# Kernel optimization log

Measured on AMD Instinct MI355X. Metric: run time of the kernel, lower is better.

The kernel has to match this reference:

```python
import jax, jax.numpy as jnp
import numpy as np

N_NODES = 50000
N_EDGES = 1000000
NODE_F = 64
EDGE_F = 64
OUT_F = 128
K = 2  # matches init k=2


def setup_inputs() -> dict:
    key = jax.random.key(0)
    k1, k2, k3, k4, k5, k6 = jax.random.split(key, 6)
    node_feat = jax.random.normal(k1, (N_NODES, NODE_F), dtype=jnp.float32)
    edge_feat = jax.random.normal(k2, (N_EDGES, EDGE_F), dtype=jnp.float32)
    # nn.Linear(edge_feats*2 + node_feats, out_feats): weight [out, in], bias [out]
    W = jax.random.normal(k3, (OUT_F, 2 * EDGE_F + NODE_F), dtype=jnp.float32) * 0.05
    b = jax.random.normal(k4, (OUT_F,), dtype=jnp.float32) * 0.05
    src = jax.random.randint(k5, (N_EDGES,), 0, N_NODES, dtype=jnp.int64)
    dst = jax.random.randint(k6, (N_EDGES,), 0, N_NODES, dtype=jnp.int64)
    return {"node_feat": node_feat, "edge_feat": edge_feat, "W": W, "b": b,
            "src": src, "dst": dst}


def reference(node_feat, edge_feat, W, b, src, dst):
    N = node_feat.shape[0]
    # norm = in_degrees().clamp(min=1) ** -0.5, shape [N, 1]
    deg = jax.ops.segment_sum(jnp.ones_like(dst, dtype=node_feat.dtype), dst,
                              num_segments=N)
    norm = jnp.maximum(deg, 1.0) ** -0.5
    norm = norm[:, None]
    # DGL semantics: update_all(copy_e, sum) overwrites ndata['h'] with the
    # scatter-sum of edge data over destination nodes; apply_edges then copies
    # the (un-normalized) node 'h' back to edges via edge.src.
    e = edge_feat  # [E, EDGE_F]
    fstack = [node_feat]
    for _ in range(K):
        h = jax.ops.segment_sum(e, dst, num_segments=N)  # [N, EDGE_F]
        fstack.append(h * norm)
        e = h[src]  # apply_edges: e = src node h (un-normalized)
    rst = jnp.concatenate(fstack, axis=-1) @ W.T + b  # [N, OUT_F]
    est = rst[src]  # final apply_edges copies lin output to edges
    return rst, est
```

## Files before the change

kernel.cpp:

```cpp
#include <hip/hip_runtime.h>
#include <hip/hip_bf16.h>

#define NF 64
#define N_OUT 128
#define CAT 192

typedef __attribute__((ext_vector_type(4))) float f32x4;
typedef __attribute__((ext_vector_type(8))) short bf16x8;

__device__ inline short f2bf(float x) {
  unsigned u = __float_as_uint(x);
  unsigned r = (u + 0x7fff + ((u >> 16) & 1)) >> 16;
  return (short)r;
}

__device__ inline f32x4 sx4(f32x4 v, int m) {
  f32x4 r;
  r.x = __shfl_xor(v.x, m, 64);
  r.y = __shfl_xor(v.y, m, 64);
  r.z = __shfl_xor(v.z, m, 64);
  r.w = __shfl_xor(v.w, m, 64);
  return r;
}

__global__ __launch_bounds__(256) void deg_kernel(const int* __restrict__ dst,
                                                  int* __restrict__ deg, int n_edges) {
  int i = blockIdx.x * blockDim.x + threadIdx.x;
  int stride = gridDim.x * blockDim.x;
  for (; i < n_edges; i += stride) {
    int d = __builtin_nontemporal_load(&dst[i]);
    atomicAdd(&deg[d], 1);
  }
}

__global__ __launch_bounds__(256) void scanA_kernel(const int* __restrict__ deg,
                                                    int* __restrict__ offs,
                                                    float* __restrict__ norm,
                                                    int* __restrict__ bsum, int n) {
  int tid = threadIdx.x;
  int i = blockIdx.x * 256 + tid;
  int lane = tid & 63, wid = tid >> 6;
  int v = (i < n) ? deg[i] : 0;
  int s = v;
  #pragma unroll
  for (int o = 1; o < 64; o <<= 1) {
    int t = __shfl_up(s, o, 64);
    if (lane >= o) s += t;
  }
  __shared__ int ws[4], wb[4];
  if (lane == 63) ws[wid] = s;
  __syncthreads();
  if (tid == 0) {
    int run = 0;
    #pragma unroll
    for (int w = 0; w < 4; ++w) { wb[w] = run; run += ws[w]; }
    bsum[blockIdx.x] = run;
  }
  __syncthreads();
  if (i < n) {
    offs[i] = wb[wid] + s - v;
    norm[i] = rsqrtf(fmaxf((float)v, 1.0f));
  }
}

__global__ __launch_bounds__(256) void scanBC_kernel(const int* __restrict__ bsum,
                                                     int* __restrict__ offs, int n, int nb) {
  int tid = threadIdx.x, lane = tid & 63, wid = tid >> 6;
  int v = (tid < nb) ? bsum[tid] : 0;
  int s = v;
  #pragma unroll
  for (int o = 1; o < 64; o <<= 1) {
    int t = __shfl_up(s, o, 64);
    if (lane >= o) s += t;
  }
  __shared__ int ws[4], wb[4];
  if (lane == 63) ws[wid] = s;
  __syncthreads();
  if (tid == 0) {
    int run = 0;
    #pragma unroll
    for (int w = 0; w < 4; ++w) { wb[w] = run; run += ws[w]; }
  }
  __syncthreads();
  __shared__ int sbase;
  if (tid == blockIdx.x) sbase = wb[wid] + s - v;
  __syncthreads();
  int i = blockIdx.x * 256 + tid;
  if (i < n) offs[i] += sbase;
}

__global__ __launch_bounds__(256) void fill_kernel(const int* __restrict__ src,
                                                   const int* __restrict__ dst,
                                                   int* __restrict__ offs,
                                                   long long* __restrict__ csr, int n_edges) {
  int i = blockIdx.x * blockDim.x + threadIdx.x;
  int stride = gridDim.x * blockDim.x;
  for (; i < n_edges; i += stride) {
    int d = __builtin_nontemporal_load(&dst[i]);
    int s = __builtin_nontemporal_load(&src[i]);
    int p = atomicAdd(&offs[d], 1);
    long long pk = (long long)(((unsigned long long)(unsigned)s << 32) | (unsigned)i);
    __builtin_nontemporal_store(pk, &csr[p]);
  }
}

__global__ __launch_bounds__(256) void h1_kernel(const float* __restrict__ edge_feat,
                                                 const int2* __restrict__ csr,
                                                 const int* __restrict__ offs,
                                                 float* __restrict__ h1, int n_nodes) {
  int n = blockIdx.x * 4 + (threadIdx.x >> 6);
  if (n >= n_nodes) return;
  int l = threadIdx.x & 63;
  int l15 = l & 15, l4 = l >> 4;
  int kb = n ? offs[n - 1] : 0;
  int ke = offs[n];
  f32x4 acc0 = {0.f,0.f,0.f,0.f}, acc1 = {0.f,0.f,0.f,0.f};
  f32x4 acc2 = {0.f,0.f,0.f,0.f}, acc3 = {0.f,0.f,0.f,0.f};
  int k = kb;
  for (; k + 16 <= ke; k += 16) {
    int e0 = csr[k + l4].x;
    int e1 = csr[k + 4 + l4].x;
    int e2 = csr[k + 8 + l4].x;
    int e3 = csr[k + 12 + l4].x;
    acc0 += __builtin_nontemporal_load((const f32x4*)&edge_feat[(size_t)e0 * NF + l15 * 4]);
    acc1 += __builtin_nontemporal_load((const f32x4*)&edge_feat[(size_t)e1 * NF + l15 * 4]);
    acc2 += __builtin_nontemporal_load((const f32x4*)&edge_feat[(size_t)e2 * NF + l15 * 4]);
    acc3 += __builtin_nontemporal_load((const f32x4*)&edge_feat[(size_t)e3 * NF + l15 * 4]);
  }
  if (k + 8 <= ke) {
    int e0 = csr[k + l4].x;
    int e1 = csr[k + 4 + l4].x;
    acc0 += __builtin_nontemporal_load((const f32x4*)&edge_feat[(size_t)e0 * NF + l15 * 4]);
    acc1 += __builtin_nontemporal_load((const f32x4*)&edge_feat[(size_t)e1 * NF + l15 * 4]);
    k += 8;
  }
  if (k + 4 <= ke) {
    int e = csr[k + l4].x;
    acc2 += __builtin_nontemporal_load((const f32x4*)&edge_feat[(size_t)e * NF + l15 * 4]);
    k += 4;
  }
  int rem = ke - k;
  if (l4 < rem) {
    int e = csr[k + l4].x;
    acc3 += __builtin_nontemporal_load((const f32x4*)&edge_feat[(size_t)e * NF + l15 * 4]);
  }
  f32x4 t = (acc0 + acc1) + (acc2 + acc3);
  t += sx4(t, 16);
  t += sx4(t, 32);
  if (l4 == 0) *(f32x4*)&h1[(size_t)n * NF + l15 * 4] = t;
}

__global__ __launch_bounds__(256) void h2_kernel(const float* __restrict__ h1,
                                                 const int2* __restrict__ csr,
                                                 const int* __restrict__ offs,
                                                 float* __restrict__ h2, int n_nodes) {
  int n = blockIdx.x * 4 + (threadIdx.x >> 6);
  if (n >= n_nodes) return;
  int l = threadIdx.x & 63;
  int l15 = l & 15, l4 = l >> 4;
  int kb = n ? offs[n - 1] : 0;
  int ke = offs[n];
  f32x4 acc0 = {0.f,0.f,0.f,0.f}, acc1 = {0.f,0.f,0.f,0.f};
  f32x4 acc2 = {0.f,0.f,0.f,0.f}, acc3 = {0.f,0.f,0.f,0.f};
  int k = kb;
  for (; k + 16 <= ke; k += 16) {
    int s0 = csr[k + l4].y;
    int s1 = csr[k + 4 + l4].y;
    int s2 = csr[k + 8 + l4].y;
    int s3 = csr[k + 12 + l4].y;
    acc0 += *(const f32x4*)&h1[(size_t)s0 * NF + l15 * 4];
    acc1 += *(const f32x4*)&h1[(size_t)s1 * NF + l15 * 4];
    acc2 += *(const f32x4*)&h1[(size_t)s2 * NF + l15 * 4];
    acc3 += *(const f32x4*)&h1[(size_t)s3 * NF + l15 * 4];
  }
  if (k + 8 <= ke) {
    int s0 = csr[k + l4].y;
    int s1 = csr[k + 4 + l4].y;
    acc0 += *(const f32x4*)&h1[(size_t)s0 * NF + l15 * 4];
    acc1 += *(const f32x4*)&h1[(size_t)s1 * NF + l15 * 4];
    k += 8;
  }
  if (k + 4 <= ke) {
    int s = csr[k + l4].y;
    acc2 += *(const f32x4*)&h1[(size_t)s * NF + l15 * 4];
    k += 4;
  }
  int rem = ke - k;
  if (l4 < rem) {
    int s = csr[k + l4].y;
    acc3 += *(const f32x4*)&h1[(size_t)s * NF + l15 * 4];
  }
  f32x4 t = (acc0 + acc1) + (acc2 + acc3);
  t += sx4(t, 16);
  t += sx4(t, 32);
  if (l4 == 0) *(f32x4*)&h2[(size_t)n * NF + l15 * 4] = t;
}

__global__ __launch_bounds__(512) void gemm_kernel(const float* __restrict__ node_feat,
                                                   const float* __restrict__ h1,
                                                   const float* __restrict__ h2,
                                                   const float* __restrict__ norm,
                                                   const float* __restrict__ W,
                                                   const float* __restrict__ bias,
                                                   float* __restrict__ rst,
                                                   short* __restrict__ rstb, int n_nodes) {
  __shared__ short F[64 * 200];
  __shared__ float R[64][132];
  int tid = threadIdx.x;
  int l = tid & 63, w = tid >> 6;
  int w2 = w & 3, wh = w >> 2;
  int l15 = l & 15, l4 = l >> 4;

  bf16x8 Bf[6][2];
  #pragma unroll
  for (int c = 0; c < 2; ++c) {
    int col = w2 * 32 + c * 16 + l15;
    const float* wp = &W[(size_t)col * CAT];
    #pragma unroll
    for (int ks = 0; ks < 6; ++ks) {
      int k0 = ks * 32 + l4 * 8;
      bf16x8 b;
      #pragma unroll
      for (int j = 0; j < 8; ++j) b[j] = f2bf(wp[k0 + j]);
      Bf[ks][c] = b;
    }
  }
  float bias0 = bias[w2 * 32 + l15];
  float bias1 = bias[w2 * 32 + 16 + l15];

  int tiles = (n_nodes + 63) / 64;
  for (int tile = blockIdx.x; tile < tiles; tile += gridDim.x) {
    int nbase = tile * 64;
    __syncthreads();
    for (int idx = tid; idx < 1536; idx += 512) {
      int m = idx / 24, q = idx - m * 24;
      int n = nbase + m;
      bf16x8 pk;
      if (n < n_nodes) {
        const float* sp;
        float scale = 1.f;
        if (q < 8)       sp = &node_feat[(size_t)n * NF + q * 8];
        else if (q < 16) { sp = &h1[(size_t)n * NF + (q - 8) * 8]; scale = norm[n]; }
        else             { sp = &h2[(size_t)n * NF + (q - 16) * 8]; scale = norm[n]; }
        f32x4 v0 = *(const f32x4*)sp;
        f32x4 v1 = *(const f32x4*)(sp + 4);
        pk[0] = f2bf(v0.x * scale); pk[1] = f2bf(v0.y * scale);
        pk[2] = f2bf(v0.z * scale); pk[3] = f2bf(v0.w * scale);
        pk[4] = f2bf(v1.x * scale); pk[5] = f2bf(v1.y * scale);
        pk[6] = f2bf(v1.z * scale); pk[7] = f2bf(v1.w * scale);
      } else {
        pk = bf16x8{0,0,0,0,0,0,0,0};
      }
      *(bf16x8*)&F[m * 200 + q * 8] = pk;
    }
    __syncthreads();
    f32x4 acc00 = {0.f,0.f,0.f,0.f}, acc01 = {0.f,0.f,0.f,0.f};
    f32x4 acc10 = {0.f,0.f,0.f,0.f}, acc11 = {0.f,0.f,0.f,0.f};
    #pragma unroll
    for (int ks = 0; ks < 6; ++ks) {
      bf16x8 a0 = *(const bf16x8*)&F[(wh * 32 + l15) * 200 + ks * 32 + l4 * 8];
      bf16x8 a1 = *(const bf16x8*)&F[(wh * 32 + 16 + l15) * 200 + ks * 32 + l4 * 8];
      acc00 = __builtin_amdgcn_mfma_f32_16x16x32_bf16(a0, Bf[ks][0], acc00, 0, 0, 0);
      acc01 = __builtin_amdgcn_mfma_f32_16x16x32_bf16(a0, Bf[ks][1], acc01, 0, 0, 0);
      acc10 = __builtin_amdgcn_mfma_f32_16x16x32_bf16(a1, Bf[ks][0], acc10, 0, 0, 0);
      acc11 = __builtin_amdgcn_mfma_f32_16x16x32_bf16(a1, Bf[ks][1], acc11, 0, 0, 0);
    }
    #pragma unroll
    for (int rt = 0; rt < 2; ++rt) {
      f32x4 ac0 = rt ? acc10 : acc00;
      f32x4 ac1 = rt ? acc11 : acc01;
      #pragma unroll
      for (int r = 0; r < 4; ++r) {
        int row = wh * 32 + rt * 16 + l4 * 4 + r;
        R[row][w2 * 32 + l15] = ac0[r] + bias0;
        R[row][w2 * 32 + 16 + l15] = ac1[r] + bias1;
      }
    }
    __syncthreads();
    for (int idx = tid; idx < 64 * 32; idx += 512) {
      int m = idx >> 5, c = idx & 31;
      int n = nbase + m;
      if (n < n_nodes) {
        f32x4 v = *(const f32x4*)&R[m][c * 4];
        __builtin_nontemporal_store(v, (f32x4*)&rst[(size_t)n * N_OUT + c * 4]);
      }
    }
    if (rstb) {
      for (int idx = tid; idx < 64 * 16; idx += 512) {
        int m = idx >> 4, q = idx & 15;
        int n = nbase + m;
        if (n < n_nodes) {
          const float* rp = &R[m][q * 8];
          bf16x8 pk;
          #pragma unroll
          for (int j = 0; j < 8; ++j) pk[j] = f2bf(rp[j]);
          *(bf16x8*)&rstb[(size_t)n * N_OUT + q * 8] = pk;
        }
      }
    }
  }
}

__global__ __launch_bounds__(256) void est_bf16_kernel(const short* __restrict__ rstb,
                                                       const int* __restrict__ src,
                                                       float* __restrict__ est, int n_edges) {
  f32x4* e4 = (f32x4*)est;
  int total = n_edges * 32;
  int i = blockIdx.x * blockDim.x + threadIdx.x;
  int stride = gridDim.x * blockDim.x;
  for (; i < total; i += stride) {
    int e = i >> 5, c = i & 31;
    ushort4 b = *(const ushort4*)&rstb[(size_t)src[e] * N_OUT + c * 4];
    f32x4 v;
    v.x = __uint_as_float((unsigned)b.x << 16);
    v.y = __uint_as_float((unsigned)b.y << 16);
    v.z = __uint_as_float((unsigned)b.z << 16);
    v.w = __uint_as_float((unsigned)b.w << 16);
    __builtin_nontemporal_store(v, &e4[i]);
  }
}

__global__ __launch_bounds__(256) void est_f32_kernel(const float* __restrict__ rst,
                                                      const int* __restrict__ src,
                                                      float* __restrict__ est, int n_edges) {
  const f32x4* r4 = (const f32x4*)rst;
  f32x4* e4 = (f32x4*)est;
  int total = n_edges * 32;
  int i = blockIdx.x * blockDim.x + threadIdx.x;
  int stride = gridDim.x * blockDim.x;
  for (; i < total; i += stride) {
    int e = i >> 5, c = i & 31;
    f32x4 v = r4[(size_t)src[e] * 32 + c];
    __builtin_nontemporal_store(v, &e4[i]);
  }
}

extern "C" void kernel_launch(void* const* d_in, const int* in_sizes, int n_in,
                              void* d_out, int out_size, void* d_ws, size_t ws_size,
                              hipStream_t stream) {
  const float* node_feat = (const float*)d_in[0];
  const float* edge_feat = (const float*)d_in[1];
  const float* W = (const float*)d_in[2];
  const float* bias = (const float*)d_in[3];
  const int* src = (const int*)d_in[4];
  const int* dst = (const int*)d_in[5];
  int n_nodes = in_sizes[0] / NF;
  int n_edges = in_sizes[4];

  size_t off = 0;
  auto take = [&](size_t bytes) -> void* {
    void* p = (char*)d_ws + off;
    off += (bytes + 255) & ~(size_t)255;
    return p;
  };
  int* deg = (int*)take((size_t)n_nodes * 4);
  int* offs = (int*)take(((size_t)n_nodes + 1) * 4);
  float* norm = (float*)take((size_t)n_nodes * 4);
  int* bsum = (int*)take(256 * 4);
  long long* csr = (long long*)take((size_t)n_edges * 8);
  float* h1 = (float*)take((size_t)n_nodes * NF * 4);
  float* h2 = (float*)take((size_t)n_nodes * NF * 4);
  size_t rstb_bytes = (size_t)n_nodes * N_OUT * 2;
  short* rstb = nullptr;
  if (off + rstb_bytes <= ws_size) rstb = (short*)take(rstb_bytes);

  float* rst = (float*)d_out;
  float* est = rst + (size_t)n_nodes * N_OUT;

  (void)hipMemsetAsync(deg, 0, (size_t)n_nodes * 4, stream);

  deg_kernel<<<2048, 256, 0, stream>>>(dst, deg, n_edges);
  int nbs = (n_nodes + 255) / 256;
  scanA_kernel<<<nbs, 256, 0, stream>>>(deg, offs, norm, bsum, n_nodes);
  scanBC_kernel<<<nbs, 256, 0, stream>>>(bsum, offs, n_nodes, nbs);
  fill_kernel<<<2048, 256, 0, stream>>>(src, dst, offs, csr, n_edges);
  int nb = (n_nodes + 3) / 4;
  h1_kernel<<<nb, 256, 0, stream>>>(edge_feat, (const int2*)csr, offs, h1, n_nodes);
  h2_kernel<<<nb, 256, 0, stream>>>(h1, (const int2*)csr, offs, h2, n_nodes);
  gemm_kernel<<<512, 512, 0, stream>>>(node_feat, h1, h2, norm, W, bias,
                                       rst, rstb, n_nodes);
  if (rstb)
    est_bf16_kernel<<<8192, 256, 0, stream>>>(rstb, src, est, n_edges);
  else
    est_f32_kernel<<<8192, 256, 0, stream>>>(rst, src, est, n_edges);
}
```

Measured before the change: 382.8 us.

## Store intermediate node features in bf16 and prenormalize before GEMM

The first aggregation kernel now writes h1 as bf16 twice, once raw and once scaled by norm, and also converts node_feat to bf16. The second aggregation kernel gathers the bf16 raw h1 and writes a normalized bf16 h2. The GEMM then loads pre-packed bf16 tiles directly instead of converting fp32 with scaling. The goal is to halve the gather traffic in h2 and the GEMM's load bytes. In exchange, h1 is rounded to bf16 before the second aggregation, which adds error, and the fp32 fallback for est is removed, so the bf16 workspace is assumed always to fit.

```diff
diff --git a/kernel.cpp b/kernel.cpp
--- a/kernel.cpp
+++ b/kernel.cpp
@@ -8,10 +8,25 @@
 typedef __attribute__((ext_vector_type(4))) float f32x4;
 typedef __attribute__((ext_vector_type(8))) short bf16x8;
 
-__device__ inline short f2bf(float x) {
+__device__ inline unsigned short f2bf(float x) {
   unsigned u = __float_as_uint(x);
   unsigned r = (u + 0x7fff + ((u >> 16) & 1)) >> 16;
-  return (short)r;
+  return (unsigned short)r;
+}
+
+__device__ inline ushort4 pack4(f32x4 v) {
+  ushort4 r;
+  r.x = f2bf(v.x); r.y = f2bf(v.y); r.z = f2bf(v.z); r.w = f2bf(v.w);
+  return r;
+}
+
+__device__ inline f32x4 unpack4(ushort4 b) {
+  f32x4 v;
+  v.x = __uint_as_float((unsigned)b.x << 16);
+  v.y = __uint_as_float((unsigned)b.y << 16);
+  v.z = __uint_as_float((unsigned)b.z << 16);
+  v.w = __uint_as_float((unsigned)b.w << 16);
+  return v;
 }
 
 __device__ inline f32x4 sx4(f32x4 v, int m) {
@@ -105,9 +120,14 @@
 }
 
 __global__ __launch_bounds__(256) void h1_kernel(const float* __restrict__ edge_feat,
+                                                 const float* __restrict__ node_feat,
                                                  const int2* __restrict__ csr,
                                                  const int* __restrict__ offs,
-                                                 float* __restrict__ h1, int n_nodes) {
+                                                 const float* __restrict__ norm,
+                                                 unsigned short* __restrict__ h1r,
+                                                 unsigned short* __restrict__ h1n,
+                                                 unsigned short* __restrict__ nfb,
+                                                 int n_nodes) {
   int n = blockIdx.x * 4 + (threadIdx.x >> 6);
   if (n >= n_nodes) return;
   int l = threadIdx.x & 63;
@@ -147,13 +167,23 @@
   f32x4 t = (acc0 + acc1) + (acc2 + acc3);
   t += sx4(t, 16);
   t += sx4(t, 32);
-  if (l4 == 0) *(f32x4*)&h1[(size_t)n * NF + l15 * 4] = t;
-}
-
-__global__ __launch_bounds__(256) void h2_kernel(const float* __restrict__ h1,
+  if (l4 == 0) {
+    *(ushort4*)&h1r[(size_t)n * NF + l15 * 4] = pack4(t);
+    float nm = norm[n];
+    f32x4 tn = t; tn.x *= nm; tn.y *= nm; tn.z *= nm; tn.w *= nm;
+    *(ushort4*)&h1n[(size_t)n * NF + l15 * 4] = pack4(tn);
+  } else if (l4 == 1) {
+    f32x4 v = *(const f32x4*)&node_feat[(size_t)n * NF + l15 * 4];
+    *(ushort4*)&nfb[(size_t)n * NF + l15 * 4] = pack4(v);
+  }
+}
+
+__global__ __launch_bounds__(256) void h2_kernel(const unsigned short* __restrict__ h1r,
                                                  const int2* __restrict__ csr,
                                                  const int* __restrict__ offs,
-                                                 float* __restrict__ h2, int n_nodes) {
+                                                 const float* __restrict__ norm,
+                                                 unsigned short* __restrict__ h2n,
+                                                 int n_nodes) {
   int n = blockIdx.x * 4 + (threadIdx.x >> 6);
   if (n >= n_nodes) return;
   int l = threadIdx.x & 63;
@@ -168,42 +198,46 @@
     int s1 = csr[k + 4 + l4].y;
     int s2 = csr[k + 8 + l4].y;
     int s3 = csr[k + 12 + l4].y;
-    acc0 += *(const f32x4*)&h1[(size_t)s0 * NF + l15 * 4];
-    acc1 += *(const f32x4*)&h1[(size_t)s1 * NF + l15 * 4];
-    acc2 += *(const f32x4*)&h1[(size_t)s2 * NF + l15 * 4];
-    acc3 += *(const f32x4*)&h1[(size_t)s3 * NF + l15 * 4];
+    acc0 += unpack4(*(const ushort4*)&h1r[(size_t)s0 * NF + l15 * 4]);
+    acc1 += unpack4(*(const ushort4*)&h1r[(size_t)s1 * NF + l15 * 4]);
+    acc2 += unpack4(*(const ushort4*)&h1r[(size_t)s2 * NF + l15 * 4]);
+    acc3 += unpack4(*(const ushort4*)&h1r[(size_t)s3 * NF + l15 * 4]);
   }
   if (k + 8 <= ke) {
     int s0 = csr[k + l4].y;
     int s1 = csr[k + 4 + l4].y;
-    acc0 += *(const f32x4*)&h1[(size_t)s0 * NF + l15 * 4];
-    acc1 += *(const f32x4*)&h1[(size_t)s1 * NF + l15 * 4];
+    acc0 += unpack4(*(const ushort4*)&h1r[(size_t)s0 * NF + l15 * 4]);
+    acc1 += unpack4(*(const ushort4*)&h1r[(size_t)s1 * NF + l15 * 4]);
     k += 8;
   }
   if (k + 4 <= ke) {
     int s = csr[k + l4].y;
-    acc2 += *(const f32x4*)&h1[(size_t)s * NF + l15 * 4];
+    acc2 += unpack4(*(const ushort4*)&h1r[(size_t)s * NF + l15 * 4]);
     k += 4;
   }
   int rem = ke - k;
   if (l4 < rem) {
     int s = csr[k + l4].y;
-    acc3 += *(const f32x4*)&h1[(size_t)s * NF + l15 * 4];
+    acc3 += unpack4(*(const ushort4*)&h1r[(size_t)s * NF + l15 * 4]);
   }
   f32x4 t = (acc0 + acc1) + (acc2 + acc3);
   t += sx4(t, 16);
   t += sx4(t, 32);
-  if (l4 == 0) *(f32x4*)&h2[(size_t)n * NF + l15 * 4] = t;
-}
-
-__global__ __launch_bounds__(512) void gemm_kernel(const float* __restrict__ node_feat,
-                                                   const float* __restrict__ h1,
-                                                   const float* __restrict__ h2,
-                                                   const float* __restrict__ norm,
+  if (l4 == 0) {
+    float nm = norm[n];
+    t.x *= nm; t.y *= nm; t.z *= nm; t.w *= nm;
+    *(ushort4*)&h2n[(size_t)n * NF + l15 * 4] = pack4(t);
+  }
+}
+
+__global__ __launch_bounds__(512) void gemm_kernel(const unsigned short* __restrict__ nfb,
+                                                   const unsigned short* __restrict__ h1n,
+                                                   const unsigned short* __restrict__ h2n,
                                                    const float* __restrict__ W,
                                                    const float* __restrict__ bias,
                                                    float* __restrict__ rst,
-                                                   short* __restrict__ rstb, int n_nodes) {
+                                                   unsigned short* __restrict__ rstb,
+                                                   int n_nodes) {
   __shared__ short F[64 * 200];
   __shared__ float R[64][132];
   int tid = threadIdx.x;
@@ -221,7 +255,7 @@
       int k0 = ks * 32 + l4 * 8;
       bf16x8 b;
       #pragma unroll
-      for (int j = 0; j < 8; ++j) b[j] = f2bf(wp[k0 + j]);
+      for (int j = 0; j < 8; ++j) b[j] = (short)f2bf(wp[k0 + j]);
       Bf[ks][c] = b;
     }
   }
@@ -235,21 +269,10 @@
     for (int idx = tid; idx < 1536; idx += 512) {
       int m = idx / 24, q = idx - m * 24;
       int n = nbase + m;
-      bf16x8 pk;
+      bf16x8 pk = bf16x8{0,0,0,0,0,0,0,0};
       if (n < n_nodes) {
-        const float* sp;
-        float scale = 1.f;
-        if (q < 8)       sp = &node_feat[(size_t)n * NF + q * 8];
-        else if (q < 16) { sp = &h1[(size_t)n * NF + (q - 8) * 8]; scale = norm[n]; }
-        else             { sp = &h2[(size_t)n * NF + (q - 16) * 8]; scale = norm[n]; }
-        f32x4 v0 = *(const f32x4*)sp;
-        f32x4 v1 = *(const f32x4*)(sp + 4);
-        pk[0] = f2bf(v0.x * scale); pk[1] = f2bf(v0.y * scale);
-        pk[2] = f2bf(v0.z * scale); pk[3] = f2bf(v0.w * scale);
-        pk[4] = f2bf(v1.x * scale); pk[5] = f2bf(v1.y * scale);
-        pk[6] = f2bf(v1.z * scale); pk[7] = f2bf(v1.w * scale);
-      } else {
-        pk = bf16x8{0,0,0,0,0,0,0,0};
+        const unsigned short* base = (q < 8) ? nfb : (q < 16) ? h1n : h2n;
+        pk = *(const bf16x8*)&base[(size_t)n * NF + (q & 7) * 8];
       }
       *(bf16x8*)&F[m * 200 + q * 8] = pk;
     }
@@ -285,23 +308,21 @@
         __builtin_nontemporal_store(v, (f32x4*)&rst[(size_t)n * N_OUT + c * 4]);
       }
     }
-    if (rstb) {
-      for (int idx = tid; idx < 64 * 16; idx += 512) {
-        int m = idx >> 4, q = idx & 15;
-        int n = nbase + m;
-        if (n < n_nodes) {
-          const float* rp = &R[m][q * 8];
-          bf16x8 pk;
-          #pragma unroll
-          for (int j = 0; j < 8; ++j) pk[j] = f2bf(rp[j]);
-          *(bf16x8*)&rstb[(size_t)n * N_OUT + q * 8] = pk;
-        }
+    for (int idx = tid; idx < 64 * 16; idx += 512) {
+      int m = idx >> 4, q = idx & 15;
+      int n = nbase + m;
+      if (n < n_nodes) {
+        const float* rp = &R[m][q * 8];
+        bf16x8 pk;
+        #pragma unroll
+        for (int j = 0; j < 8; ++j) pk[j] = (short)f2bf(rp[j]);
+        *(bf16x8*)&rstb[(size_t)n * N_OUT + q * 8] = pk;
       }
     }
   }
 }
 
-__global__ __launch_bounds__(256) void est_bf16_kernel(const short* __restrict__ rstb,
+__global__ __launch_bounds__(256) void est_bf16_kernel(const unsigned short* __restrict__ rstb,
                                                        const int* __restrict__ src,
                                                        float* __restrict__ est, int n_edges) {
   f32x4* e4 = (f32x4*)est;
@@ -311,27 +332,7 @@
   for (; i < total; i += stride) {
     int e = i >> 5, c = i & 31;
     ushort4 b = *(const ushort4*)&rstb[(size_t)src[e] * N_OUT + c * 4];
-    f32x4 v;
-    v.x = __uint_as_float((unsigned)b.x << 16);
-    v.y = __uint_as_float((unsigned)b.y << 16);
-    v.z = __uint_as_float((unsigned)b.z << 16);
-    v.w = __uint_as_float((unsigned)b.w << 16);
-    __builtin_nontemporal_store(v, &e4[i]);
-  }
-}
-
-__global__ __launch_bounds__(256) void est_f32_kernel(const float* __restrict__ rst,
-                                                      const int* __restrict__ src,
-                                                      float* __restrict__ est, int n_edges) {
-  const f32x4* r4 = (const f32x4*)rst;
-  f32x4* e4 = (f32x4*)est;
-  int total = n_edges * 32;
-  int i = blockIdx.x * blockDim.x + threadIdx.x;
-  int stride = gridDim.x * blockDim.x;
-  for (; i < total; i += stride) {
-    int e = i >> 5, c = i & 31;
-    f32x4 v = r4[(size_t)src[e] * 32 + c];
-    __builtin_nontemporal_store(v, &e4[i]);
+    __builtin_nontemporal_store(unpack4(b), &e4[i]);
   }
 }
 
@@ -358,11 +359,11 @@
   float* norm = (float*)take((size_t)n_nodes * 4);
   int* bsum = (int*)take(256 * 4);
   long long* csr = (long long*)take((size_t)n_edges * 8);
-  float* h1 = (float*)take((size_t)n_nodes * NF * 4);
-  float* h2 = (float*)take((size_t)n_nodes * NF * 4);
-  size_t rstb_bytes = (size_t)n_nodes * N_OUT * 2;
-  short* rstb = nullptr;
-  if (off + rstb_bytes <= ws_size) rstb = (short*)take(rstb_bytes);
+  unsigned short* h1r = (unsigned short*)take((size_t)n_nodes * NF * 2);
+  unsigned short* h1n = (unsigned short*)take((size_t)n_nodes * NF * 2);
+  unsigned short* h2n = (unsigned short*)take((size_t)n_nodes * NF * 2);
+  unsigned short* nfb = (unsigned short*)take((size_t)n_nodes * NF * 2);
+  unsigned short* rstb = (unsigned short*)take((size_t)n_nodes * N_OUT * 2);
 
   float* rst = (float*)d_out;
   float* est = rst + (size_t)n_nodes * N_OUT;
@@ -375,12 +376,9 @@
   scanBC_kernel<<<nbs, 256, 0, stream>>>(bsum, offs, n_nodes, nbs);
   fill_kernel<<<2048, 256, 0, stream>>>(src, dst, offs, csr, n_edges);
   int nb = (n_nodes + 3) / 4;
-  h1_kernel<<<nb, 256, 0, stream>>>(edge_feat, (const int2*)csr, offs, h1, n_nodes);
-  h2_kernel<<<nb, 256, 0, stream>>>(h1, (const int2*)csr, offs, h2, n_nodes);
-  gemm_kernel<<<512, 512, 0, stream>>>(node_feat, h1, h2, norm, W, bias,
-                                       rst, rstb, n_nodes);
-  if (rstb)
-    est_bf16_kernel<<<8192, 256, 0, stream>>>(rstb, src, est, n_edges);
-  else
-    est_f32_kernel<<<8192, 256, 0, stream>>>(rst, src, est, n_edges);
-}
+  h1_kernel<<<nb, 256, 0, stream>>>(edge_feat, node_feat, (const int2*)csr, offs,
+                                    norm, h1r, h1n, nfb, n_nodes);
+  h2_kernel<<<nb, 256, 0, stream>>>(h1r, (const int2*)csr, offs, norm, h2n, n_nodes);
+  gemm_kernel<<<512, 512, 0, stream>>>(nfb, h1n, h2n, W, bias, rst, rstb, n_nodes);
+  est_bf16_kernel<<<8192, 256, 0, stream>>>(rstb, src, est, n_edges);
+}
```

Result: no change. 381.1 us (-0.4%).
